# Kernel optimization log

Hardware: AMD Instinct MI355X
Metric: run time of the kernel (lower is better)

Reference implementation:

```python
import jax, jax.numpy as jnp
import numpy as np

DN = ('NCHW', 'OIHW', 'NCHW')
EPS = 1e-5


def _mask_time(x, lengths):
    # zero out positions t >= length along the last (time) axis
    T = x.shape[-1]
    valid = jnp.arange(T)[None, None, None, :] < lengths[:, None, None, None]
    return jnp.where(valid, x, jnp.zeros((), x.dtype))


def _conv(x, w, b, stride, pad):
    y = jax.lax.conv_general_dilated(x, w, window_strides=stride,
                                     padding=[(pad[0], pad[0]), (pad[1], pad[1])],
                                     dimension_numbers=DN)
    return y + b[None, :, None, None]


def _bn(x, g, be, m, v):
    inv = jax.lax.rsqrt(v + EPS)
    return (x - m[None, :, None, None]) * (g * inv)[None, :, None, None] + be[None, :, None, None]


def setup_inputs() -> dict:
    key = jax.random.key(0)
    ks = jax.random.split(key, 16)
    f32 = jnp.float32
    return {
        'x': jax.random.normal(ks[0], (16, 1, 161, 1024), f32),
        'x_lengths': jax.random.randint(ks[1], (16,), 1, 512),
        'w1': jax.random.normal(ks[2], (32, 1, 41, 11), f32) * 0.05,
        'b1': jax.random.normal(ks[3], (32,), f32) * 0.05,
        'g1': jax.random.uniform(ks[4], (32,), f32) + 0.5,
        'be1': jax.random.normal(ks[5], (32,), f32) * 0.05,
        'm1': jax.random.normal(ks[6], (32,), f32) * 0.05,
        'v1': jax.random.uniform(ks[7], (32,), f32) + 0.5,
        'w2': jax.random.normal(ks[8], (32, 32, 21, 11), f32) * 0.02,
        'b2': jax.random.normal(ks[9], (32,), f32) * 0.05,
        'g2': jax.random.uniform(ks[10], (32,), f32) + 0.5,
        'be2': jax.random.normal(ks[11], (32,), f32) * 0.05,
        'm2': jax.random.normal(ks[12], (32,), f32) * 0.05,
        'v2': jax.random.uniform(ks[13], (32,), f32) + 0.5,
    }


def reference(x, x_lengths, w1, b1, g1, be1, m1, v1, w2, b2, g2, be2, m2, v2):
    # module 1: conv1 -> mask
    h = _mask_time(_conv(x, w1, b1, (2, 2), (20, 5)), x_lengths)   # [16,32,81,512]
    # module 2: bn1 -> mask
    h = _mask_time(_bn(h, g1, be1, m1, v1), x_lengths)
    # module 3: hardtanh(0,20) -> mask
    h = _mask_time(jnp.clip(h, 0.0, 20.0), x_lengths)
    # module 4: conv2 -> mask
    h = _mask_time(_conv(h, w2, b2, (2, 1), (10, 5)), x_lengths)   # [16,32,41,512]
    # module 5: bn2 -> mask
    h = _mask_time(_bn(h, g2, be2, m2, v2), x_lengths)
    # module 6: hardtanh(0,20) -> mask
    h = _mask_time(jnp.clip(h, 0.0, 20.0), x_lengths)
    return h
```

## Files before the change

kernel.cpp:

```cpp
#include <hip/hip_runtime.h>

typedef __attribute__((ext_vector_type(8))) __bf16 bf16x8;
typedef __attribute__((ext_vector_type(16))) float f32x16;

__device__ __forceinline__ unsigned short f2bf(float f) {
    unsigned int u = __float_as_uint(f);
    unsigned int r = (u + 0x7FFFu + ((u >> 16) & 1u)) >> 16;
    return (unsigned short)r;
}

#define GLL16(gp, lp) \
    __builtin_amdgcn_global_load_lds( \
        (const __attribute__((address_space(1))) unsigned int*)(gp), \
        (__attribute__((address_space(3))) unsigned int*)(lp), 16, 0, 0)

__global__ __launch_bounds__(256) void prep_w1t(const float* __restrict__ w1,
                                                unsigned short* __restrict__ w1t)
{
    const int t = blockIdx.x * 256 + threadIdx.x;
    const int k    = t % 48;
    const int rest = t / 48;
    const int oc   = rest & 31;
    const int kw   = rest >> 5;
    unsigned short v = 0;
    if (k < 41) v = f2bf(w1[(oc * 41 + k) * 11 + kw]);
    w1t[t] = v;
}

__global__ __launch_bounds__(256) void prep_w2f(const float* __restrict__ w2,
                                                unsigned short* __restrict__ w2tf)
{
    const int gid = blockIdx.x * 256 + threadIdx.x;
    const int j  = gid & 7;
    const int l  = (gid >> 3) & 63;
    const int s  = (gid >> 9) & 1;
    const int ti = gid >> 10;
    const int khp = ti / 11;
    const int kw  = ti - khp * 11;
    const int kh  = khp - 2;
    const int oc  = l & 31;
    const int ic  = s * 16 + ((l >> 5) << 3) + j;
    unsigned short v = 0;
    if ((unsigned)kh <= 20u)
        v = f2bf(w2[((oc * 32 + ic) * 21 + kh) * 11 + kw]);
    w2tf[gid] = v;
}

__global__ __launch_bounds__(256) void zero_halo(unsigned short* __restrict__ h1s)
{
    const int id  = blockIdx.x * 256 + threadIdx.x;
    const int c16 = id & 15;
    const int q   = (id >> 4) & 3;
    const int nr  = id >> 6;
    const int c   = c16 < 5 ? c16 : 512 + c16;
    uint4 z = {0u, 0u, 0u, 0u};
    *(uint4*)((char*)h1s + ((size_t)(nr * 4 + q) * 528 + c) * 16) = z;
}

__global__ __launch_bounds__(256) void conv1_mfma(
    const float* __restrict__ x, const int* __restrict__ xlen,
    const unsigned short* __restrict__ w1t,
    const float* __restrict__ b1, const float* __restrict__ g1,
    const float* __restrict__ be1, const float* __restrict__ m1,
    const float* __restrict__ v1,
    unsigned short* __restrict__ h1s)
{
    __shared__ uint4 lds4[2128];
    char* lds = (char*)lds4;

    const int t  = threadIdx.x;
    const int bx = blockIdx.x;
    const int yi = blockIdx.y;
    const int n  = blockIdx.z;
    const int oh0 = ((yi >> 2) << 3) + (yi & 3);
    const int len = xlen[n];

    const int l   = t & 63;
    const int w   = t >> 6;
    const int l31 = l & 31;
    const int lhi = l >> 5;

    char* h8 = (char*)h1s;
    const size_t rowpitch = 33792;

    if (bx * 128 >= len) {
        #pragma unroll
        for (int it = 0; it < 4; ++it) {
            const int idx = t + it * 256;
            const int d1 = idx >> 9;
            const int q  = (idx >> 7) & 3;
            const int cl = idx & 127;
            const int oh = oh0 + 4 * d1;
            if (oh <= 80) {
                uint4 z = {0u, 0u, 0u, 0u};
                *(uint4*)(h8 + (size_t)(n * 81 + oh) * rowpitch + q * 8448
                          + (5 + (bx << 7) + cl) * 16) = z;
            }
        }
        return;
    }

    const int cw   = t & 63;
    const int jrow = t >> 6;
    const int gr0  = 2 * oh0 - 20;
    const int gc0  = bx * 256 - 5;
    const float* xn = x + (size_t)n * 161 * 1024;
    #pragma unroll
    for (int cg = 0; cg < 5; ++cg) {
        const int c = cg * 64 + cw;
        if (c < 266) {
            const int gc = gc0 + c;
            const bool cok = (gc >= 0) && (gc < 1024);
            #pragma unroll
            for (int jj = 0; jj < 2; ++jj) {
                const int j = jrow + 4 * jj;
                if (j < 7) {
                    unsigned int u[4];
                    #pragma unroll
                    for (int q = 0; q < 4; ++q) {
                        const int rA = gr0 + 8 * j + 2 * q;
                        float lo = 0.f, hi = 0.f;
                        if (cok && rA >= 0 && rA < 161)         lo = xn[(size_t)rA * 1024 + gc];
                        if (cok && rA + 1 >= 0 && rA + 1 < 161) hi = xn[(size_t)(rA + 1) * 1024 + gc];
                        u[q] = (unsigned int)f2bf(lo) | ((unsigned int)f2bf(hi) << 16);
                    }
                    uint4 val; val.x = u[0]; val.y = u[1]; val.z = u[2]; val.w = u[3];
                    *(uint4*)(lds + c * 128 + ((j ^ ((c >> 1) & 7)) << 4)) = val;
                }
            }
        }
    }
    __syncthreads();

    const int i = (w << 5) + l31;

    f32x16 acc0 = {}, acc1 = {};
    const char* w1tb = (const char*)w1t;
    #pragma unroll
    for (int kw = 0; kw < 11; ++kw) {
        const char* ap = w1tb + kw * 3072 + l31 * 96 + lhi * 16;
        const bf16x8 a0 = *(const bf16x8*)(ap);
        const bf16x8 a1 = *(const bf16x8*)(ap + 32);
        const bf16x8 a2 = *(const bf16x8*)(ap + 64);
        const int c = 2 * i + kw;
        const char* cb = lds + c * 128;
        const int sw = (c >> 1) & 7;
        const bf16x8 b00 = *(const bf16x8*)(cb + (((0 + lhi) ^ sw) << 4));
        const bf16x8 b01 = *(const bf16x8*)(cb + (((2 + lhi) ^ sw) << 4));
        const bf16x8 b02 = *(const bf16x8*)(cb + (((4 + lhi) ^ sw) << 4));
        const bf16x8 b10 = *(const bf16x8*)(cb + (((1 + lhi) ^ sw) << 4));
        const bf16x8 b11 = *(const bf16x8*)(cb + (((3 + lhi) ^ sw) << 4));
        const bf16x8 b12 = *(const bf16x8*)(cb + (((5 + lhi) ^ sw) << 4));
        acc0 = __builtin_amdgcn_mfma_f32_32x32x16_bf16(a0, b00, acc0, 0, 0, 0);
        acc0 = __builtin_amdgcn_mfma_f32_32x32x16_bf16(a1, b01, acc0, 0, 0, 0);
        acc0 = __builtin_amdgcn_mfma_f32_32x32x16_bf16(a2, b02, acc0, 0, 0, 0);
        acc1 = __builtin_amdgcn_mfma_f32_32x32x16_bf16(a0, b10, acc1, 0, 0, 0);
        acc1 = __builtin_amdgcn_mfma_f32_32x32x16_bf16(a1, b11, acc1, 0, 0, 0);
        acc1 = __builtin_amdgcn_mfma_f32_32x32x16_bf16(a2, b12, acc1, 0, 0, 0);
    }

    __syncthreads();
    const int ow  = bx * 128 + i;
    const bool vmask = ow < len;
    #pragma unroll
    for (int d1 = 0; d1 < 2; ++d1) {
        const int oh = oh0 + 4 * d1;
        if (oh <= 80) {
            #pragma unroll
            for (int q = 0; q < 4; ++q) {
                float vv[4];
                #pragma unroll
                for (int rr = 0; rr < 4; ++rr) {
                    const int reg = (q << 2) + rr;
                    const int oc  = rr + (q << 3) + (lhi << 2);
                    const float s = g1[oc] * rsqrtf(v1[oc] + 1e-5f);
                    float val = ((d1 ? acc1[reg] : acc0[reg]) + b1[oc] - m1[oc]) * s + be1[oc];
                    val = fminf(fmaxf(val, 0.f), 20.f);
                    vv[rr] = vmask ? val : 0.f;
                }
                uint2 pk;
                pk.x = (unsigned int)f2bf(vv[0]) | ((unsigned int)f2bf(vv[1]) << 16);
                pk.y = (unsigned int)f2bf(vv[2]) | ((unsigned int)f2bf(vv[3]) << 16);
                *(uint2*)(lds + (((d1 << 2) + q) << 11) + i * 16 + lhi * 8) = pk;
            }
        }
    }
    __syncthreads();
    #pragma unroll
    for (int it = 0; it < 4; ++it) {
        const int idx = t + it * 256;
        const int d1 = idx >> 9;
        const int q  = (idx >> 7) & 3;
        const int cl = idx & 127;
        const int oh = oh0 + 4 * d1;
        if (oh <= 80) {
            const uint4 v = *(const uint4*)(lds + (((d1 << 2) + q) << 11) + cl * 16);
            *(uint4*)(h8 + (size_t)(n * 81 + oh) * rowpitch + q * 8448
                      + (5 + (bx << 7) + cl) * 16) = v;
        }
    }
}

__global__ __launch_bounds__(256, 2) void conv2_v4(
    const unsigned short* __restrict__ h1s, const unsigned short* __restrict__ w2tf,
    const int* __restrict__ xlen,
    const float* __restrict__ b2, const float* __restrict__ g2,
    const float* __restrict__ be2, const float* __restrict__ m2,
    const float* __restrict__ v2, float* __restrict__ out)
{
    __shared__ char lbuf[2][20480];

    const int t   = threadIdx.x;
    const int w   = t >> 6;
    const int l   = t & 63;
    const int l31 = l & 31;
    const int lhi = l >> 5;

    const int bid = blockIdx.x;
    const int lb  = (bid & 7) * 84 + (bid >> 3);
    const int bx  = lb & 1;
    const int rest = lb >> 1;
    const int by  = rest % 21;
    const int n   = rest / 21;

    const int ow0 = bx << 8;
    const int len = xlen[n];

    if (ow0 >= len) {
        #pragma unroll
        for (int j = 0; j < 2; ++j) {
            const int oh2 = 2 * by + j;
            if (oh2 <= 40) {
                #pragma unroll
                for (int g = 0; g < 2; ++g) {
                    const int ow = ow0 + (w << 6) + (g << 5) + l31;
                    #pragma unroll
                    for (int reg = 0; reg < 16; ++reg) {
                        const int oc = (reg & 3) + ((reg >> 2) << 3) + (lhi << 2);
                        out[((size_t)(n * 32 + oc) * 41 + oh2) * 512 + ow] = 0.f;
                    }
                }
            }
        }
        return;
    }

    const int rlo = (4 * by - 10 > 0) ? 4 * by - 10 : 0;
    const int rhi = (4 * by + 12 < 80) ? 4 * by + 12 : 80;

    f32x16 acc[2][2] = {};

    const char* h8 = (const char*)h1s;
    const size_t rowpitch = 33792;
    const char* nb = h8 + (size_t)(n * 81) * rowpitch + (size_t)(ow0 << 4);

    #define STAGE(r, buf) do { \
        const char* g_ = nb + (size_t)(r) * rowpitch; \
        char* d_ = &lbuf[buf][0]; \
        _Pragma("unroll") \
        for (int pl_ = 0; pl_ < 4; ++pl_) \
            GLL16(g_ + pl_ * 8448 + t * 16, d_ + pl_ * 5120 + t * 16); \
        GLL16(g_ + w * 8448 + 4096 + (t & 63) * 16, \
              d_ + w * 5120 + 4096 + (t & 63) * 16); \
    } while (0)

    STAGE(rlo, 0);
    __syncthreads();

    int cur = 0;
    for (int r = rlo; r <= rhi; ++r) {
        if (r < rhi) STAGE(r + 1, cur ^ 1);
        const char* lb8 = &lbuf[cur][0];
        const int khb = r - 4 * by + 10;
        const char* w8v = (const char*)w2tf;
        #pragma unroll
        for (int kw = 0; kw < 11; ++kw) {
            const int cbase = (w << 6) + kw + l31;
            #pragma unroll
            for (int s = 0; s < 2; ++s) {
                const char* bp = lb8 + (2 * s + lhi) * 5120 + cbase * 16;
                const bf16x8 B0 = *(const bf16x8*)(bp);
                const bf16x8 B1 = *(const bf16x8*)(bp + 512);
                #pragma unroll
                for (int j = 0; j < 2; ++j) {
                    const int khp = khb + 2 - 2 * j;
                    const bf16x8 A = *(const bf16x8*)(w8v
                        + (size_t)(((khp * 11 + kw) * 2 + s) << 10) + (l << 4));
                    acc[j][0] = __builtin_amdgcn_mfma_f32_32x32x16_bf16(A, B0, acc[j][0], 0, 0, 0);
                    acc[j][1] = __builtin_amdgcn_mfma_f32_32x32x16_bf16(A, B1, acc[j][1], 0, 0, 0);
                }
            }
        }
        __syncthreads();
        cur ^= 1;
    }

    #pragma unroll
    for (int j = 0; j < 2; ++j) {
        const int oh2 = 2 * by + j;
        if (oh2 <= 40) {
            #pragma unroll
            for (int g = 0; g < 2; ++g) {
                const int ow = ow0 + (w << 6) + (g << 5) + l31;
                const bool valid = ow < len;
                #pragma unroll
                for (int reg = 0; reg < 16; ++reg) {
                    const int oc = (reg & 3) + ((reg >> 2) << 3) + (lhi << 2);
                    const float s = g2[oc] * rsqrtf(v2[oc] + 1e-5f);
                    float val = (acc[j][g][reg] + b2[oc] - m2[oc]) * s + be2[oc];
                    val = fminf(fmaxf(val, 0.f), 20.f);
                    if (!valid) val = 0.f;
                    out[((size_t)(n * 32 + oc) * 41 + oh2) * 512 + ow] = val;
                }
            }
        }
    }
}

extern "C" void kernel_launch(void* const* d_in, const int* in_sizes, int n_in,
                              void* d_out, int out_size, void* d_ws, size_t ws_size,
                              hipStream_t stream) {
    const float* x    = (const float*)d_in[0];
    const int*   xlen = (const int*)  d_in[1];
    const float* w1   = (const float*)d_in[2];
    const float* b1   = (const float*)d_in[3];
    const float* g1   = (const float*)d_in[4];
    const float* be1  = (const float*)d_in[5];
    const float* m1   = (const float*)d_in[6];
    const float* v1   = (const float*)d_in[7];
    const float* w2   = (const float*)d_in[8];
    const float* b2   = (const float*)d_in[9];
    const float* g2   = (const float*)d_in[10];
    const float* be2  = (const float*)d_in[11];
    const float* m2   = (const float*)d_in[12];
    const float* v2   = (const float*)d_in[13];
    float* out = (float*)d_out;

    unsigned short* h1s  = (unsigned short*)d_ws;
    unsigned short* w2tf = h1s + 21897216;
    unsigned short* w1t  = w2tf + 281600;

    prep_w1t<<<dim3(66),   dim3(256), 0, stream>>>(w1, w1t);
    prep_w2f<<<dim3(1100), dim3(256), 0, stream>>>(w2, w2tf);
    zero_halo<<<dim3(324), dim3(256), 0, stream>>>(h1s);
    conv1_mfma<<<dim3(4, 41, 16), dim3(256), 0, stream>>>(
        x, xlen, w1t, b1, g1, be1, m1, v1, h1s);
    conv2_v4<<<dim3(672), dim3(256), 0, stream>>>(
        h1s, w2tf, xlen, b2, g2, be2, m2, v2, out);
}
```

Measured before the change: 229.3 us.

## Split conv2 tiles narrower and divide channel halves across waves with LDS reduction

```diff
diff --git a/kernel.cpp b/kernel.cpp
--- a/kernel.cpp
+++ b/kernel.cpp
@@ -201,44 +201,45 @@
     }
 }
 
-__global__ __launch_bounds__(256, 2) void conv2_v4(
+__global__ __launch_bounds__(256, 2) void conv2_v5(
     const unsigned short* __restrict__ h1s, const unsigned short* __restrict__ w2tf,
     const int* __restrict__ xlen,
     const float* __restrict__ b2, const float* __restrict__ g2,
     const float* __restrict__ be2, const float* __restrict__ m2,
     const float* __restrict__ v2, float* __restrict__ out)
 {
-    __shared__ char lbuf[2][20480];
+    __shared__ char lbuf[32768];
 
     const int t   = threadIdx.x;
     const int w   = t >> 6;
     const int l   = t & 63;
     const int l31 = l & 31;
     const int lhi = l >> 5;
-
-    const int bid = blockIdx.x;
-    const int lb  = (bid & 7) * 84 + (bid >> 3);
-    const int bx  = lb & 1;
-    const int rest = lb >> 1;
-    const int by  = rest % 21;
-    const int n   = rest / 21;
-
-    const int ow0 = bx << 8;
+    const int cg  = w >> 1;
+    const int s   = w & 1;
+
+    const int bid  = blockIdx.x;
+    const int lb   = (bid & 7) * 168 + (bid >> 3);
+    const int n    = lb / 84;
+    const int r2   = lb - n * 84;
+    const int by   = r2 >> 2;
+    const int bx   = r2 & 3;
+
+    const int ow0 = bx << 7;
     const int len = xlen[n];
 
     if (ow0 >= len) {
-        #pragma unroll
-        for (int j = 0; j < 2; ++j) {
-            const int oh2 = 2 * by + j;
-            if (oh2 <= 40) {
-                #pragma unroll
-                for (int g = 0; g < 2; ++g) {
-                    const int ow = ow0 + (w << 6) + (g << 5) + l31;
-                    #pragma unroll
-                    for (int reg = 0; reg < 16; ++reg) {
-                        const int oc = (reg & 3) + ((reg >> 2) << 3) + (lhi << 2);
-                        out[((size_t)(n * 32 + oc) * 41 + oh2) * 512 + ow] = 0.f;
-                    }
+        const int j   = w >> 1;
+        const int cgz = w & 1;
+        const int oh2 = 2 * by + j;
+        if (oh2 <= 40) {
+            #pragma unroll
+            for (int g = 0; g < 2; ++g) {
+                const int ow = ow0 + (cgz << 6) + (g << 5) + l31;
+                #pragma unroll
+                for (int reg = 0; reg < 16; ++reg) {
+                    const int oc = (reg & 3) + ((reg >> 2) << 3) + (lhi << 2);
+                    out[((size_t)(n * 32 + oc) * 41 + oh2) * 512 + ow] = 0.f;
                 }
             }
         }
@@ -255,59 +256,81 @@
     const char* nb = h8 + (size_t)(n * 81) * rowpitch + (size_t)(ow0 << 4);
 
     #define STAGE(r, buf) do { \
-        const char* g_ = nb + (size_t)(r) * rowpitch; \
-        char* d_ = &lbuf[buf][0]; \
-        _Pragma("unroll") \
-        for (int pl_ = 0; pl_ < 4; ++pl_) \
-            GLL16(g_ + pl_ * 8448 + t * 16, d_ + pl_ * 5120 + t * 16); \
-        GLL16(g_ + w * 8448 + 4096 + (t & 63) * 16, \
-              d_ + w * 5120 + 4096 + (t & 63) * 16); \
+        const char* g_ = nb + (size_t)(r) * rowpitch + w * 8448; \
+        char* d_ = lbuf + (buf) * 9216 + w * 2304; \
+        GLL16(g_ + l * 16,        d_ + l * 16); \
+        GLL16(g_ + 1024 + l * 16, d_ + 1024 + l * 16); \
+        if (l < 16) GLL16(g_ + 2048 + l * 16, d_ + 2048 + l * 16); \
     } while (0)
 
     STAGE(rlo, 0);
     __syncthreads();
 
+    const char* w8v = (const char*)w2tf;
     int cur = 0;
     for (int r = rlo; r <= rhi; ++r) {
         if (r < rhi) STAGE(r + 1, cur ^ 1);
-        const char* lb8 = &lbuf[cur][0];
+        const char* lb8 = lbuf + cur * 9216;
         const int khb = r - 4 * by + 10;
-        const char* w8v = (const char*)w2tf;
         #pragma unroll
         for (int kw = 0; kw < 11; ++kw) {
-            const int cbase = (w << 6) + kw + l31;
-            #pragma unroll
-            for (int s = 0; s < 2; ++s) {
-                const char* bp = lb8 + (2 * s + lhi) * 5120 + cbase * 16;
-                const bf16x8 B0 = *(const bf16x8*)(bp);
-                const bf16x8 B1 = *(const bf16x8*)(bp + 512);
-                #pragma unroll
-                for (int j = 0; j < 2; ++j) {
-                    const int khp = khb + 2 - 2 * j;
-                    const bf16x8 A = *(const bf16x8*)(w8v
-                        + (size_t)(((khp * 11 + kw) * 2 + s) << 10) + (l << 4));
-                    acc[j][0] = __builtin_amdgcn_mfma_f32_32x32x16_bf16(A, B0, acc[j][0], 0, 0, 0);
-                    acc[j][1] = __builtin_amdgcn_mfma_f32_32x32x16_bf16(A, B1, acc[j][1], 0, 0, 0);
-                }
+            const char* bp = lb8 + (2 * s + lhi) * 2304 + ((cg << 6) + l31 + kw) * 16;
+            const bf16x8 B0 = *(const bf16x8*)(bp);
+            const bf16x8 B1 = *(const bf16x8*)(bp + 512);
+            #pragma unroll
+            for (int j = 0; j < 2; ++j) {
+                const int khp = khb + 2 - 2 * j;
+                const bf16x8 A = *(const bf16x8*)(w8v
+                    + (size_t)(((khp * 11 + kw) * 2 + s) << 10) + (l << 4));
+                acc[j][0] = __builtin_amdgcn_mfma_f32_32x32x16_bf16(A, B0, acc[j][0], 0, 0, 0);
+                acc[j][1] = __builtin_amdgcn_mfma_f32_32x32x16_bf16(A, B1, acc[j][1], 0, 0, 0);
             }
         }
         __syncthreads();
         cur ^= 1;
     }
+    #undef STAGE
+
+    if (s == 1) {
+        #pragma unroll
+        for (int j = 0; j < 2; ++j) {
+            #pragma unroll
+            for (int f = 0; f < 2; ++f) {
+                char* dst = lbuf + ((((cg << 1) + j) << 1) + f) * 4096 + l * 16;
+                #pragma unroll
+                for (int q = 0; q < 4; ++q) {
+                    float4 v;
+                    v.x = acc[j][f][q * 4 + 0]; v.y = acc[j][f][q * 4 + 1];
+                    v.z = acc[j][f][q * 4 + 2]; v.w = acc[j][f][q * 4 + 3];
+                    *(float4*)(dst + q * 1024) = v;
+                }
+            }
+        }
+    }
+    __syncthreads();
+    if (s == 1) return;
 
     #pragma unroll
     for (int j = 0; j < 2; ++j) {
         const int oh2 = 2 * by + j;
         if (oh2 <= 40) {
             #pragma unroll
-            for (int g = 0; g < 2; ++g) {
-                const int ow = ow0 + (w << 6) + (g << 5) + l31;
+            for (int f = 0; f < 2; ++f) {
+                const char* src = lbuf + ((((cg << 1) + j) << 1) + f) * 4096 + l * 16;
+                float pr[16];
+                #pragma unroll
+                for (int q = 0; q < 4; ++q) {
+                    const float4 v = *(const float4*)(src + q * 1024);
+                    pr[q * 4 + 0] = v.x; pr[q * 4 + 1] = v.y;
+                    pr[q * 4 + 2] = v.z; pr[q * 4 + 3] = v.w;
+                }
+                const int ow = ow0 + (cg << 6) + (f << 5) + l31;
                 const bool valid = ow < len;
                 #pragma unroll
                 for (int reg = 0; reg < 16; ++reg) {
                     const int oc = (reg & 3) + ((reg >> 2) << 3) + (lhi << 2);
-                    const float s = g2[oc] * rsqrtf(v2[oc] + 1e-5f);
-                    float val = (acc[j][g][reg] + b2[oc] - m2[oc]) * s + be2[oc];
+                    const float sc = g2[oc] * rsqrtf(v2[oc] + 1e-5f);
+                    float val = (acc[j][f][reg] + pr[reg] + b2[oc] - m2[oc]) * sc + be2[oc];
                     val = fminf(fmaxf(val, 0.f), 20.f);
                     if (!valid) val = 0.f;
                     out[((size_t)(n * 32 + oc) * 41 + oh2) * 512 + ow] = val;
@@ -345,6 +368,6 @@
     zero_halo<<<dim3(324), dim3(256), 0, stream>>>(h1s);
     conv1_mfma<<<dim3(4, 41, 16), dim3(256), 0, stream>>>(
         x, xlen, w1t, b1, g1, be1, m1, v1, h1s);
-    conv2_v4<<<dim3(672), dim3(256), 0, stream>>>(
+    conv2_v5<<<dim3(1344), dim3(256), 0, stream>>>(
         h1s, w2tf, xlen, b2, g2, be2, m2, v2, out);
 }
```

Measured after the change: 220.4 us. 1.04x faster.

## Compute four output rows per conv2 block to reuse staged input rows

Applied to the files above, without the earlier changes.

```diff
diff --git a/kernel.cpp b/kernel.cpp
--- a/kernel.cpp
+++ b/kernel.cpp
@@ -37,7 +37,7 @@
     const int ti = gid >> 10;
     const int khp = ti / 11;
     const int kw  = ti - khp * 11;
-    const int kh  = khp - 2;
+    const int kh  = khp - 6;
     const int oc  = l & 31;
     const int ic  = s * 16 + ((l >> 5) << 3) + j;
     unsigned short v = 0;
@@ -201,14 +201,14 @@
     }
 }
 
-__global__ __launch_bounds__(256, 2) void conv2_v4(
+__global__ __launch_bounds__(256, 2) void conv2_v6(
     const unsigned short* __restrict__ h1s, const unsigned short* __restrict__ w2tf,
     const int* __restrict__ xlen,
     const float* __restrict__ b2, const float* __restrict__ g2,
     const float* __restrict__ be2, const float* __restrict__ m2,
     const float* __restrict__ v2, float* __restrict__ out)
 {
-    __shared__ char lbuf[2][20480];
+    __shared__ char lbuf[2][17408];
 
     const int t   = threadIdx.x;
     const int w   = t >> 6;
@@ -217,23 +217,23 @@
     const int lhi = l >> 5;
 
     const int bid = blockIdx.x;
-    const int lb  = (bid & 7) * 84 + (bid >> 3);
-    const int bx  = lb & 1;
-    const int rest = lb >> 1;
-    const int by  = rest % 21;
-    const int n   = rest / 21;
+    const int lb  = (bid * 181) % 352;
+    const int n   = lb / 22;
+    const int rr  = lb - n * 22;
+    const int by  = rr >> 1;
+    const int bx  = rr & 1;
 
     const int ow0 = bx << 8;
     const int len = xlen[n];
 
     if (ow0 >= len) {
         #pragma unroll
-        for (int j = 0; j < 2; ++j) {
-            const int oh2 = 2 * by + j;
+        for (int j = 0; j < 4; ++j) {
+            const int oh2 = 4 * by + j;
             if (oh2 <= 40) {
                 #pragma unroll
-                for (int g = 0; g < 2; ++g) {
-                    const int ow = ow0 + (w << 6) + (g << 5) + l31;
+                for (int f = 0; f < 2; ++f) {
+                    const int ow = ow0 + (w << 6) + (f << 5) + l31;
                     #pragma unroll
                     for (int reg = 0; reg < 16; ++reg) {
                         const int oc = (reg & 3) + ((reg >> 2) << 3) + (lhi << 2);
@@ -245,45 +245,43 @@
         return;
     }
 
-    const int rlo = (4 * by - 10 > 0) ? 4 * by - 10 : 0;
-    const int rhi = (4 * by + 12 < 80) ? 4 * by + 12 : 80;
-
-    f32x16 acc[2][2] = {};
-
-    const char* h8 = (const char*)h1s;
-    const size_t rowpitch = 33792;
-    const char* nb = h8 + (size_t)(n * 81) * rowpitch + (size_t)(ow0 << 4);
+    const int rlo = (8 * by - 10 > 0) ? 8 * by - 10 : 0;
+    const int rhi = (8 * by + 16 < 80) ? 8 * by + 16 : 80;
+
+    f32x16 acc[4][2] = {};
+
+    const char* nb = (const char*)h1s + (size_t)(n * 81) * 33792 + (size_t)(ow0 << 4);
 
     #define STAGE(r, buf) do { \
-        const char* g_ = nb + (size_t)(r) * rowpitch; \
-        char* d_ = &lbuf[buf][0]; \
-        _Pragma("unroll") \
-        for (int pl_ = 0; pl_ < 4; ++pl_) \
-            GLL16(g_ + pl_ * 8448 + t * 16, d_ + pl_ * 5120 + t * 16); \
-        GLL16(g_ + w * 8448 + 4096 + (t & 63) * 16, \
-              d_ + w * 5120 + 4096 + (t & 63) * 16); \
+        const char* g_ = nb + (size_t)(r) * 33792 + w * 8448; \
+        char* d_ = &lbuf[buf][0] + w * 4352; \
+        GLL16(g_ + l * 16,        d_ + l * 16); \
+        GLL16(g_ + 1024 + l * 16, d_ + 1024 + l * 16); \
+        GLL16(g_ + 2048 + l * 16, d_ + 2048 + l * 16); \
+        GLL16(g_ + 3072 + l * 16, d_ + 3072 + l * 16); \
+        if (l < 16) GLL16(g_ + 4096 + l * 16, d_ + 4096 + l * 16); \
     } while (0)
 
     STAGE(rlo, 0);
     __syncthreads();
 
+    const char* w8v = (const char*)w2tf;
     int cur = 0;
     for (int r = rlo; r <= rhi; ++r) {
         if (r < rhi) STAGE(r + 1, cur ^ 1);
         const char* lb8 = &lbuf[cur][0];
-        const int khb = r - 4 * by + 10;
-        const char* w8v = (const char*)w2tf;
+        const int khb6 = r - 8 * by + 16;
         #pragma unroll
         for (int kw = 0; kw < 11; ++kw) {
-            const int cbase = (w << 6) + kw + l31;
+            const int cb = (w << 6) + kw + l31;
             #pragma unroll
             for (int s = 0; s < 2; ++s) {
-                const char* bp = lb8 + (2 * s + lhi) * 5120 + cbase * 16;
+                const char* bp = lb8 + (2 * s + lhi) * 4352 + cb * 16;
                 const bf16x8 B0 = *(const bf16x8*)(bp);
                 const bf16x8 B1 = *(const bf16x8*)(bp + 512);
                 #pragma unroll
-                for (int j = 0; j < 2; ++j) {
-                    const int khp = khb + 2 - 2 * j;
+                for (int j = 0; j < 4; ++j) {
+                    const int khp = khb6 - 2 * j;
                     const bf16x8 A = *(const bf16x8*)(w8v
                         + (size_t)(((khp * 11 + kw) * 2 + s) << 10) + (l << 4));
                     acc[j][0] = __builtin_amdgcn_mfma_f32_32x32x16_bf16(A, B0, acc[j][0], 0, 0, 0);
@@ -294,20 +292,21 @@
         __syncthreads();
         cur ^= 1;
     }
-
-    #pragma unroll
-    for (int j = 0; j < 2; ++j) {
-        const int oh2 = 2 * by + j;
+    #undef STAGE
+
+    #pragma unroll
+    for (int j = 0; j < 4; ++j) {
+        const int oh2 = 4 * by + j;
         if (oh2 <= 40) {
             #pragma unroll
-            for (int g = 0; g < 2; ++g) {
-                const int ow = ow0 + (w << 6) + (g << 5) + l31;
+            for (int f = 0; f < 2; ++f) {
+                const int ow = ow0 + (w << 6) + (f << 5) + l31;
                 const bool valid = ow < len;
                 #pragma unroll
                 for (int reg = 0; reg < 16; ++reg) {
                     const int oc = (reg & 3) + ((reg >> 2) << 3) + (lhi << 2);
-                    const float s = g2[oc] * rsqrtf(v2[oc] + 1e-5f);
-                    float val = (acc[j][g][reg] + b2[oc] - m2[oc]) * s + be2[oc];
+                    const float sc = g2[oc] * rsqrtf(v2[oc] + 1e-5f);
+                    float val = (acc[j][f][reg] + b2[oc] - m2[oc]) * sc + be2[oc];
                     val = fminf(fmaxf(val, 0.f), 20.f);
                     if (!valid) val = 0.f;
                     out[((size_t)(n * 32 + oc) * 41 + oh2) * 512 + ow] = val;
@@ -338,13 +337,13 @@
 
     unsigned short* h1s  = (unsigned short*)d_ws;
     unsigned short* w2tf = h1s + 21897216;
-    unsigned short* w1t  = w2tf + 281600;
+    unsigned short* w1t  = w2tf + 743424;
 
     prep_w1t<<<dim3(66),   dim3(256), 0, stream>>>(w1, w1t);
-    prep_w2f<<<dim3(1100), dim3(256), 0, stream>>>(w2, w2tf);
+    prep_w2f<<<dim3(2904), dim3(256), 0, stream>>>(w2, w2tf);
     zero_halo<<<dim3(324), dim3(256), 0, stream>>>(h1s);
     conv1_mfma<<<dim3(4, 41, 16), dim3(256), 0, stream>>>(
         x, xlen, w1t, b1, g1, be1, m1, v1, h1s);
-    conv2_v4<<<dim3(672), dim3(256), 0, stream>>>(
+    conv2_v6<<<dim3(352), dim3(256), 0, stream>>>(
         h1s, w2tf, xlen, b2, g2, be2, m2, v2, out);
 }
```

New measurement: 318.4 us. 38.9% more time.
